# Performance work log

Measured on AMD Instinct MI355X. Metric: run time of the kernel, lower is better.

Reference implementation:

```python
import jax, jax.numpy as jnp
import numpy as np

H = 256
NUM_HEADS = 4
HEAD_DIM = H // NUM_HEADS


def _mlp(x, W1, b1, W2, b2):
    # Linear(2H->H) + ReLU + (dropout=identity in eval) + Linear(H->H)
    h = jax.nn.relu(x @ W1.T + b1)
    return h @ W2.T + b2


def setup_inputs() -> dict:
    key = jax.random.key(0)
    ks = jax.random.split(key, 24)
    s2h = 1.0 / np.sqrt(2 * H)
    sh = 1.0 / np.sqrt(H)
    inp = {
        'qubit_embeddings': jax.random.normal(ks[0], (65536, H), jnp.float32),
        'qpu_embeddings': jax.random.normal(ks[1], (64, H), jnp.float32),
        'gate_embeddings': jax.random.normal(ks[2], (65536, H), jnp.float32),
        'all_embeddings': jax.random.normal(ks[3], (131072, H), jnp.float32),
        'time_table': jax.random.normal(ks[4], (1000, H), jnp.float32),
        'map_W1': jax.random.normal(ks[5], (H, 2 * H), jnp.float32) * s2h,
        'map_b1': jnp.zeros((H,), jnp.float32),
        'map_W2': jax.random.normal(ks[6], (H, H), jnp.float32) * sh,
        'map_b2': jnp.zeros((H,), jnp.float32),
        'sch_W1': jax.random.normal(ks[7], (H, 2 * H), jnp.float32) * s2h,
        'sch_b1': jnp.zeros((H,), jnp.float32),
        'sch_W2': jax.random.normal(ks[8], (H, H), jnp.float32) * sh,
        'sch_b2': jnp.zeros((H,), jnp.float32),
        'qg_W1': jax.random.normal(ks[9], (H, H), jnp.float32) * sh,
        'qg_b1': jnp.zeros((H,), jnp.float32),
        'qg_W2': jax.random.normal(ks[10], (H, H), jnp.float32) * sh,
        'qg_b2': jnp.zeros((H,), jnp.float32),
        'attn_Wq': jax.random.normal(ks[11], (H, H), jnp.float32) * sh,
        'attn_bq': jnp.zeros((H,), jnp.float32),
        'attn_Wk': jax.random.normal(ks[12], (H, H), jnp.float32) * sh,
        'attn_bk': jnp.zeros((H,), jnp.float32),
        'attn_Wv': jax.random.normal(ks[13], (H, H), jnp.float32) * sh,
        'attn_bv': jnp.zeros((H,), jnp.float32),
        'attn_Wo': jax.random.normal(ks[14], (H, H), jnp.float32) * sh,
        'attn_bo': jnp.zeros((H,), jnp.float32),
        'map_qubit': jax.random.randint(ks[15], (131072,), 0, 65536, jnp.int32),
        'map_qpu': jax.random.randint(ks[16], (131072,), 0, 64, jnp.int32),
        'sched_gate': jax.random.randint(ks[17], (131072,), 0, 65536, jnp.int32),
        'sched_time': jax.random.randint(ks[18], (131072,), 0, 1000, jnp.int32),
    }
    return inp


def reference(qubit_embeddings, qpu_embeddings, gate_embeddings, all_embeddings,
              time_table, map_W1, map_b1, map_W2, map_b2,
              sch_W1, sch_b1, sch_W2, sch_b2,
              qg_W1, qg_b1, qg_W2, qg_b2,
              attn_Wq, attn_bq, attn_Wk, attn_bk, attn_Wv, attn_bv,
              attn_Wo, attn_bo,
              map_qubit, map_qpu, sched_gate, sched_time):
    # Vectorized form of the per-action Python loop: gather + concat + MLP.
    map_in = jnp.concatenate([qubit_embeddings[map_qubit], qpu_embeddings[map_qpu]], axis=-1)  # [Nm, 2H]
    map_keys = _mlp(map_in, map_W1, map_b1, map_W2, map_b2)                                    # [Nm, H]
    sch_in = jnp.concatenate([gate_embeddings[sched_gate], time_table[sched_time]], axis=-1)   # [Ns, 2H]
    sch_keys = _mlp(sch_in, sch_W1, sch_b1, sch_W2, sch_b2)                                    # [Ns, H]
    keys = jnp.concatenate([map_keys, sch_keys], axis=0)                                       # [A, H]

    g = all_embeddings.mean(axis=0)                                                            # [H]
    query = jax.nn.relu(g @ qg_W1.T + qg_b1) @ qg_W2.T + qg_b2                                 # [H]

    # MultiheadAttention: batch=1, q_len=1, kv_len=A (dropout=0 in eval, mask all-valid).
    q = (query @ attn_Wq.T + attn_bq).reshape(NUM_HEADS, HEAD_DIM)
    k = (keys @ attn_Wk.T + attn_bk).reshape(-1, NUM_HEADS, HEAD_DIM)
    v = (keys @ attn_Wv.T + attn_bv).reshape(-1, NUM_HEADS, HEAD_DIM)
    scores = jnp.einsum('hd,ahd->ha', q, k) / jnp.sqrt(jnp.asarray(HEAD_DIM, q.dtype))
    w = jax.nn.softmax(scores, axis=-1)                                                        # [heads, A]
    ctx = jnp.einsum('ha,ahd->hd', w, v).reshape(H)
    attn_out = ctx @ attn_Wo.T + attn_bo                                                       # [H]

    action_logits = keys @ attn_out                                                            # [A]
    action_probs = jax.nn.softmax(action_logits, axis=-1)
    return action_probs, action_logits
```

## Files before the change

kernel.cpp:

```cpp
#include <hip/hip_runtime.h>
#include <cstdint>
#include <cstddef>

typedef __bf16 bf16_t;
typedef __bf16 bf16x8 __attribute__((ext_vector_type(8)));
typedef __bf16 bf16x4 __attribute__((ext_vector_type(4)));
typedef __bf16 bf16x2 __attribute__((ext_vector_type(2)));
typedef float f32x4 __attribute__((ext_vector_type(4)));

#define A_TOTAL 262144
#define NMAP    131072

__global__ __launch_bounds__(256) void k_w1b16(
    const float* __restrict__ mW1, const float* __restrict__ sW1,
    bf16_t* __restrict__ dst) {
  int e = blockIdx.x * 256 + threadIdx.x;
  int slice = e >> 16, idx = e & 65535;
  int n = idx >> 8, k = idx & 255;
  float v;
  switch (slice) {
    case 0:  v = mW1[n * 512 + k]; break;
    case 1:  v = mW1[n * 512 + 256 + k]; break;
    case 2:  v = sW1[n * 512 + k]; break;
    default: v = sW1[n * 512 + 256 + k]; break;
  }
  dst[e] = (bf16_t)v;
}

__global__ __launch_bounds__(256) void k_w2ext(
    const float* __restrict__ mW2, const float* __restrict__ sW2,
    bf16_t* __restrict__ wext) {
  int row = blockIdx.x, tab = blockIdx.y, k = threadIdx.x;
  const float* W2 = tab ? sW2 : mW2;
  bf16_t v = (row < 256) ? (bf16_t)W2[row * 256 + k] : (bf16_t)0.f;
  wext[(size_t)tab * 272 * 256 + (size_t)row * 256 + k] = v;
}

__global__ __launch_bounds__(256) void k_mean(const float* __restrict__ A,
                                              float* __restrict__ part) {
  int t = threadIdx.x, b = blockIdx.x;
  const float* base = A + (size_t)b * 512 * 256 + t;
  float s = 0.f;
  for (int r = 0; r < 512; ++r) s += base[(size_t)r * 256];
  part[b * 256 + t] = s;
}

__global__ __launch_bounds__(256) void k_front(
    const float* __restrict__ meanPart,
    const float* __restrict__ qgW1, const float* __restrict__ qgb1,
    const float* __restrict__ qgW2, const float* __restrict__ qgb2,
    const float* __restrict__ Wq,  const float* __restrict__ bq,
    const float* __restrict__ Wk,
    const float* __restrict__ mW2, const float* __restrict__ sW2,
    bf16_t* __restrict__ wext) {
  __shared__ float g[256], h1[256], qry[256], qv[256];
  __shared__ float qks[4][256];
  int t = threadIdx.x;
  float s = 0.f;
  for (int b = 0; b < 256; ++b) s += meanPart[b * 256 + t];
  g[t] = s * (1.0f / 131072.0f);
  __syncthreads();
  {
    const f32x4* row = (const f32x4*)(qgW1 + (size_t)t * 256);
    float acc = 0.f;
    for (int k = 0; k < 64; ++k) {
      f32x4 w = row[k];
      acc += w[0] * g[4 * k] + w[1] * g[4 * k + 1] + w[2] * g[4 * k + 2] + w[3] * g[4 * k + 3];
    }
    h1[t] = fmaxf(acc + qgb1[t], 0.f);
  }
  __syncthreads();
  {
    const f32x4* row = (const f32x4*)(qgW2 + (size_t)t * 256);
    float acc = 0.f;
    for (int k = 0; k < 64; ++k) {
      f32x4 w = row[k];
      acc += w[0] * h1[4 * k] + w[1] * h1[4 * k + 1] + w[2] * h1[4 * k + 2] + w[3] * h1[4 * k + 3];
    }
    qry[t] = acc + qgb2[t];
  }
  __syncthreads();
  {
    const f32x4* row = (const f32x4*)(Wq + (size_t)t * 256);
    float acc = 0.f;
    for (int k = 0; k < 64; ++k) {
      f32x4 w = row[k];
      acc += w[0] * qry[4 * k] + w[1] * qry[4 * k + 1] + w[2] * qry[4 * k + 2] + w[3] * qry[4 * k + 3];
    }
    qv[t] = acc + bq[t];
  }
  __syncthreads();
  for (int h = 0; h < 4; ++h) {
    float acc = 0.f;
    for (int d = 0; d < 64; ++d) acc += qv[h * 64 + d] * Wk[(size_t)(h * 64 + d) * 256 + t];
    qks[h][t] = acc * 0.125f;
  }
  __syncthreads();
  for (int tab = 0; tab < 2; ++tab) {
    const float* W2 = tab ? sW2 : mW2;
    float acc0 = 0.f, acc1 = 0.f, acc2 = 0.f, acc3 = 0.f;
    for (int n = 0; n < 256; ++n) {
      float wv = W2[(size_t)n * 256 + t];
      acc0 += qks[0][n] * wv;
      acc1 += qks[1][n] * wv;
      acc2 += qks[2][n] * wv;
      acc3 += qks[3][n] * wv;
    }
    bf16_t* dst = wext + (size_t)tab * 272 * 256;
    dst[(256 + 0) * 256 + t] = (bf16_t)acc0;
    dst[(256 + 1) * 256 + t] = (bf16_t)acc1;
    dst[(256 + 2) * 256 + t] = (bf16_t)acc2;
    dst[(256 + 3) * 256 + t] = (bf16_t)acc3;
  }
}

__global__ __launch_bounds__(512, 4) void gemm_direct3(
    const float* __restrict__ A0, int M0, const bf16_t* __restrict__ W0,
    const float* __restrict__ b0, bf16_t* __restrict__ C0, int split,
    const float* __restrict__ A1, int M1, const bf16_t* __restrict__ W1,
    const float* __restrict__ b1, bf16_t* __restrict__ C1) {
  __shared__ __align__(16) bf16_t Xo[128][264];
  int blk = blockIdx.x;
  const float* A; int M; const bf16_t* W; const float* bias; bf16_t* C; int bid;
  if (blk < split) { A = A0; M = M0; W = W0; bias = b0; C = C0; bid = blk; }
  else             { A = A1; M = M1; W = W1; bias = b1; C = C1; bid = blk - split; }
  int t = threadIdx.x;
  int w = t >> 6, lane = t & 63;
  int lm = lane & 15, q = lane >> 4;
  int mloc0 = (w & 1) * 64;
  int m0 = bid * 128 + mloc0;
  int c0 = (w >> 1) * 64;
  int rows[4];
#pragma unroll
  for (int i = 0; i < 4; ++i) {
    int m = m0 + i * 16 + lm;
    rows[i] = m < M ? m : M - 1;
  }
  f32x4 acc[4][4] = {};
#pragma unroll
  for (int kt = 0; kt < 8; ++kt) {
    int k0 = kt * 32 + q * 8;
    bf16x8 b[4];
#pragma unroll
    for (int j = 0; j < 4; ++j)
      b[j] = *(const bf16x8*)(W + (size_t)(c0 + j * 16 + lm) * 256 + k0);
#pragma unroll
    for (int i = 0; i < 4; ++i) {
      const float* src = A + (size_t)rows[i] * 256 + k0;
      f32x4 lo = *(const f32x4*)src;
      f32x4 hi = *(const f32x4*)(src + 4);
      bf16x8 a;
#pragma unroll
      for (int x = 0; x < 4; ++x) { a[x] = (bf16_t)lo[x]; a[x + 4] = (bf16_t)hi[x]; }
#pragma unroll
      for (int j = 0; j < 4; ++j)
        acc[i][j] = __builtin_amdgcn_mfma_f32_16x16x32_bf16(a, b[j], acc[i][j], 0, 0, 0);
    }
  }
#pragma unroll
  for (int j = 0; j < 4; ++j) {
    int col = c0 + j * 16 + lm;
    float bb = bias ? bias[col] : 0.f;
#pragma unroll
    for (int i = 0; i < 4; ++i)
#pragma unroll
      for (int r = 0; r < 4; ++r)
        Xo[mloc0 + i * 16 + q * 4 + r][col] = (bf16_t)(acc[i][j][r] + bb);
  }
  __syncthreads();
  size_t tile0 = (size_t)bid * 128;
  const char* lds = (const char*)&Xo[0][0];
#pragma unroll
  for (int s = 0; s < 8; ++s) {
    int flat = s * 8192 + t * 16;
    int row = flat >> 9, colb = flat & 511;
    if (tile0 + (size_t)row < (size_t)M) {
      uint4 v = *(const uint4*)(lds + row * 528 + colb);
      *(uint4*)((char*)C + tile0 * 512 + (size_t)flat) = v;
    }
  }
}

__global__ __launch_bounds__(256, 4) void gemm_gather3(
    const bf16_t* __restrict__ Pa0, const bf16_t* __restrict__ Pb0,
    const int* __restrict__ idxA0, const int* __restrict__ idxB0,
    const bf16_t* __restrict__ Wext0, const float* __restrict__ bias0,
    const bf16_t* __restrict__ Pa1, const bf16_t* __restrict__ Pb1,
    const int* __restrict__ idxA1, const int* __restrict__ idxB1,
    const bf16_t* __restrict__ Wext1, const float* __restrict__ bias1,
    bf16_t* __restrict__ C,
    float* __restrict__ scores, float* __restrict__ partMax) {
  __shared__ __align__(16) bf16_t X[64][264];
  __shared__ float sred[4];
  int blk = blockIdx.x;
  int half = blk >> 11, bid = blk & 2047;
  const bf16_t* Pa; const bf16_t* Pb; const int* idxA; const int* idxB;
  const bf16_t* Wext; const float* bias;
  if (half == 0) { Pa = Pa0; Pb = Pb0; idxA = idxA0; idxB = idxB0; Wext = Wext0; bias = bias0; }
  else           { Pa = Pa1; Pb = Pb1; idxA = idxA1; idxB = idxB1; Wext = Wext1; bias = bias1; }
  int scoreBase = half * NMAP;
  int pmBase = half * 2048;

  int t = threadIdx.x;
  int w = t >> 6, lane = t & 63;
  int lm = lane & 15, q = lane >> 4;
  int cw = w * 64;
  int r = t >> 2, qa = t & 3;
  int row0 = bid * 64;
  int ia = idxA[row0 + r], ib = idxB[row0 + r];
  const bf16_t* paRow = Pa + (size_t)ia * 256;
  const bf16_t* pbRow = Pb + (size_t)ib * 256;

  bf16x8 va[8], vb[8];
#pragma unroll
  for (int s = 0; s < 8; ++s) {
    int ch = s * 4 + qa;
    va[s] = *(const bf16x8*)(paRow + ch * 8);
    vb[s] = *(const bf16x8*)(pbRow + ch * 8);
  }
#pragma unroll
  for (int s = 0; s < 8; ++s) {
    int ch = s * 4 + qa;
    bf16x8 x;
#pragma unroll
    for (int e = 0; e < 8; ++e)
      x[e] = (bf16_t)fmaxf((float)va[s][e] + (float)vb[s][e], 0.f);
    *(bf16x8*)&X[r][ch * 8] = x;
  }
  __syncthreads();

  f32x4 acc[4][4] = {};
  f32x4 accs[4] = {};
  bool doScore = (w == 0);
#pragma unroll
  for (int kt = 0; kt < 8; ++kt) {
    int kl = kt * 32 + q * 8;
    bf16x8 a[4];
#pragma unroll
    for (int i = 0; i < 4; ++i)
      a[i] = *(const bf16x8*)&X[i * 16 + lm][kl];
#pragma unroll
    for (int j = 0; j < 4; ++j) {
      bf16x8 b = *(const bf16x8*)(Wext + (size_t)(cw + j * 16 + lm) * 256 + kl);
#pragma unroll
      for (int i = 0; i < 4; ++i)
        acc[i][j] = __builtin_amdgcn_mfma_f32_16x16x32_bf16(a[i], b, acc[i][j], 0, 0, 0);
    }
    if (doScore) {
      bf16x8 bs = *(const bf16x8*)(Wext + (size_t)(256 + lm) * 256 + kl);
#pragma unroll
      for (int i = 0; i < 4; ++i)
        accs[i] = __builtin_amdgcn_mfma_f32_16x16x32_bf16(a[i], bs, accs[i], 0, 0, 0);
    }
  }
  __syncthreads();
#pragma unroll
  for (int j = 0; j < 4; ++j) {
    int col = cw + j * 16 + lm;
    float bb = bias[col];
#pragma unroll
    for (int i = 0; i < 4; ++i)
#pragma unroll
      for (int rr = 0; rr < 4; ++rr)
        X[i * 16 + q * 4 + rr][col] = (bf16_t)(acc[i][j][rr] + bb);
  }
  float hmax = -3.4e38f;
  if (doScore) {
    if (lm < 4) {
#pragma unroll
      for (int i = 0; i < 4; ++i)
#pragma unroll
        for (int rr = 0; rr < 4; ++rr) {
          int m = i * 16 + q * 4 + rr;
          float v = accs[i][rr];
          scores[(size_t)lm * A_TOTAL + scoreBase + row0 + m] = v;
          hmax = fmaxf(hmax, v);
        }
    }
    float m1 = fmaxf(hmax, __shfl_xor(hmax, 16));
    float m2 = fmaxf(m1, __shfl_xor(m1, 32));
    if (lane < 4) sred[lane] = m2;
  }
  __syncthreads();
  size_t gRow0 = (size_t)(half * NMAP + row0);
  const char* lds = (const char*)&X[0][0];
#pragma unroll
  for (int s = 0; s < 8; ++s) {
    int flat = s * 4096 + t * 16;
    int row = flat >> 9, colb = flat & 511;
    uint4 v = *(const uint4*)(lds + row * 528 + colb);
    *(uint4*)((char*)C + gRow0 * 512 + (size_t)flat) = v;
  }
  if (t < 4) partMax[t * 4096 + pmBase + bid] = sred[t];
}

__global__ __launch_bounds__(256) void k_smax2(const float* __restrict__ pM,
                                               float* __restrict__ Mh) {
  int t = threadIdx.x;
  __shared__ float red[256];
  for (int h = 0; h < 4; ++h) {
    float m = -3.4e38f;
    for (int i = t; i < 4096; i += 256) m = fmaxf(m, pM[h * 4096 + i]);
    red[t] = m;
    __syncthreads();
    for (int s = 128; s > 0; s >>= 1) {
      if (t < s) red[t] = fmaxf(red[t], red[t + s]);
      __syncthreads();
    }
    if (t == 0) Mh[h] = red[0];
    __syncthreads();
  }
}

__global__ __launch_bounds__(256) void k_ssum(const float* __restrict__ scores,
                                              const float* __restrict__ Mh,
                                              float* __restrict__ part) {
  int b = blockIdx.x, t = threadIdx.x;
  float m = Mh[b >> 6];
  const float* base = scores + (size_t)b * 4096;
  float s = 0.f;
  for (int i = 0; i < 16; ++i) s += __expf(base[i * 256 + t] - m);
  __shared__ float red[256];
  red[t] = s;
  __syncthreads();
  for (int st = 128; st > 0; st >>= 1) {
    if (t < st) red[t] += red[t + st];
    __syncthreads();
  }
  if (t == 0) part[b] = red[0];
}

__global__ __launch_bounds__(256) void k_ssum2(const float* __restrict__ part,
                                               float* __restrict__ invS) {
  int t = threadIdx.x;
  __shared__ float red[256];
  red[t] = part[t];
  __syncthreads();
  for (int s = 32; s > 0; s >>= 1) {
    if ((t & 63) < s) red[t] += red[t + s];
    __syncthreads();
  }
  if ((t & 63) == 0) invS[t >> 6] = 1.0f / red[t];
}

__global__ __launch_bounds__(256) void k_u(
    const bf16_t* __restrict__ keys, const float* __restrict__ scores,
    const float* __restrict__ Mh, const float* __restrict__ invS,
    float* __restrict__ u) {
  __shared__ float wl[4][512];
  __shared__ float uloc[8][4][256];
  int t = threadIdx.x;
  int a0 = blockIdx.x * 512;
#pragma unroll
  for (int i = 0; i < 8; ++i) {
    int e = i * 256 + t;
    int h = e >> 9, rr = e & 511;
    wl[h][rr] = __expf(scores[(size_t)h * A_TOTAL + a0 + rr] - Mh[h]) * invS[h];
  }
  __syncthreads();
  int tc = t & 31, rh = t >> 5;
  float acc[4][8] = {};
  for (int rr = 0; rr < 64; ++rr) {
    int al = rh * 64 + rr;
    bf16x8 kv = *(const bf16x8*)(keys + (size_t)(a0 + al) * 256 + tc * 8);
    float f[8];
#pragma unroll
    for (int e = 0; e < 8; ++e) f[e] = (float)kv[e];
#pragma unroll
    for (int h = 0; h < 4; ++h) {
      float wv = wl[h][al];
#pragma unroll
      for (int e = 0; e < 8; ++e) acc[h][e] += wv * f[e];
    }
  }
#pragma unroll
  for (int h = 0; h < 4; ++h)
#pragma unroll
    for (int e = 0; e < 8; ++e) uloc[rh][h][tc * 8 + e] = acc[h][e];
  __syncthreads();
#pragma unroll
  for (int h = 0; h < 4; ++h) {
    float v = 0.f;
#pragma unroll
    for (int g = 0; g < 8; ++g) v += uloc[g][h][t];
    atomicAdd(&u[h * 256 + t], v);
  }
}

__global__ __launch_bounds__(256) void k_attn(
    const float* __restrict__ u, const float* __restrict__ Wv,
    const float* __restrict__ bv, const float* __restrict__ Wo,
    const float* __restrict__ bo, float* __restrict__ attn_out,
    bf16_t* __restrict__ attn_pad) {
  __shared__ float ctx[256];
  int t = threadIdx.x;
  int h = t >> 6;
  const float* uh = u + h * 256;
  {
    const f32x4* row = (const f32x4*)(Wv + (size_t)t * 256);
    float acc = 0.f;
    for (int k = 0; k < 64; ++k) {
      f32x4 w = row[k];
      acc += w[0] * uh[4 * k] + w[1] * uh[4 * k + 1] + w[2] * uh[4 * k + 2] + w[3] * uh[4 * k + 3];
    }
    ctx[t] = acc + bv[t];
  }
  __syncthreads();
  {
    const f32x4* row = (const f32x4*)(Wo + (size_t)t * 256);
    float acc = 0.f;
    for (int k = 0; k < 64; ++k) {
      f32x4 w = row[k];
      acc += w[0] * ctx[4 * k] + w[1] * ctx[4 * k + 1] + w[2] * ctx[4 * k + 2] + w[3] * ctx[4 * k + 3];
    }
    float v = acc + bo[t];
    attn_out[t] = v;
    attn_pad[t] = (bf16_t)v;
#pragma unroll
    for (int i = 1; i < 16; ++i) attn_pad[i * 256 + t] = (bf16_t)0.f;
  }
}

__global__ __launch_bounds__(256) void k_logits2(
    const bf16_t* __restrict__ keys, const bf16_t* __restrict__ attn_pad,
    float* __restrict__ out_logits, float* __restrict__ blockMax) {
  int t = threadIdx.x;
  int w = t >> 6, lane = t & 63;
  int lm = lane & 15, q = lane >> 4;
  int m0 = blockIdx.x * 256 + w * 64;
  bf16x8 b[8];
#pragma unroll
  for (int kt = 0; kt < 8; ++kt)
    b[kt] = *(const bf16x8*)(attn_pad + lm * 256 + kt * 32 + q * 8);
  f32x4 acc[4] = {};
#pragma unroll
  for (int i = 0; i < 4; ++i) {
    const bf16_t* arow = keys + (size_t)(m0 + i * 16 + lm) * 256 + q * 8;
#pragma unroll
    for (int kt = 0; kt < 8; ++kt) {
      bf16x8 a = *(const bf16x8*)(arow + kt * 32);
      acc[i] = __builtin_amdgcn_mfma_f32_16x16x32_bf16(a, b[kt], acc[i], 0, 0, 0);
    }
  }
  float lmax = -3.4e38f;
  if (lm == 0) {
#pragma unroll
    for (int i = 0; i < 4; ++i) {
      *(f32x4*)(out_logits + m0 + i * 16 + q * 4) = acc[i];
#pragma unroll
      for (int rr = 0; rr < 4; ++rr) lmax = fmaxf(lmax, acc[i][rr]);
    }
  }
  float m1 = fmaxf(lmax, __shfl_xor(lmax, 16));
  float m2 = fmaxf(m1, __shfl_xor(m1, 32));
  __shared__ float red[4];
  if (lane == 0) red[w] = m2;
  __syncthreads();
  if (t == 0)
    blockMax[blockIdx.x] = fmaxf(fmaxf(red[0], red[1]), fmaxf(red[2], red[3]));
}

__global__ __launch_bounds__(256) void k_lred1(const float* __restrict__ bm,
                                               float* __restrict__ Ml) {
  int t = threadIdx.x;
  float m = -3.4e38f;
  for (int i = t; i < 1024; i += 256) m = fmaxf(m, bm[i]);
  __shared__ float red[256];
  red[t] = m;
  __syncthreads();
  for (int s = 128; s > 0; s >>= 1) {
    if (t < s) red[t] = fmaxf(red[t], red[t + s]);
    __syncthreads();
  }
  if (t == 0) Ml[0] = red[0];
}

__global__ __launch_bounds__(256) void k_lsum(const float* __restrict__ logits,
                                              const float* __restrict__ Ml,
                                              float* __restrict__ part) {
  int t = threadIdx.x, b = blockIdx.x;
  float m = Ml[0];
  float s = __expf(logits[b * 512 + t] - m) + __expf(logits[b * 512 + 256 + t] - m);
  __shared__ float red[256];
  red[t] = s;
  __syncthreads();
  for (int st = 128; st > 0; st >>= 1) {
    if (t < st) red[t] += red[t + st];
    __syncthreads();
  }
  if (t == 0) part[b] = red[0];
}

__global__ __launch_bounds__(256) void k_lred2(const float* __restrict__ part,
                                               float* __restrict__ invSl) {
  int t = threadIdx.x;
  float s = part[t] + part[t + 256];
  __shared__ float red[256];
  red[t] = s;
  __syncthreads();
  for (int st = 128; st > 0; st >>= 1) {
    if (t < st) red[t] += red[t + st];
    __syncthreads();
  }
  if (t == 0) invSl[0] = 1.0f / red[0];
}

__global__ __launch_bounds__(256) void k_probs(const float* __restrict__ logits,
                                               const float* __restrict__ Ml,
                                               const float* __restrict__ invSl,
                                               float* __restrict__ probs) {
  int i = blockIdx.x * 256 + threadIdx.x;
  probs[i] = __expf(logits[i] - Ml[0]) * invSl[0];
}

extern "C" void kernel_launch(void* const* d_in, const int* in_sizes, int n_in,
                              void* d_out, int out_size, void* d_ws, size_t ws_size,
                              hipStream_t stream) {
  const float* qubit_emb = (const float*)d_in[0];
  const float* qpu_emb   = (const float*)d_in[1];
  const float* gate_emb  = (const float*)d_in[2];
  const float* all_emb   = (const float*)d_in[3];
  const float* time_tab  = (const float*)d_in[4];
  const float* map_W1 = (const float*)d_in[5];
  const float* map_b1 = (const float*)d_in[6];
  const float* map_W2 = (const float*)d_in[7];
  const float* map_b2 = (const float*)d_in[8];
  const float* sch_W1 = (const float*)d_in[9];
  const float* sch_b1 = (const float*)d_in[10];
  const float* sch_W2 = (const float*)d_in[11];
  const float* sch_b2 = (const float*)d_in[12];
  const float* qg_W1 = (const float*)d_in[13];
  const float* qg_b1 = (const float*)d_in[14];
  const float* qg_W2 = (const float*)d_in[15];
  const float* qg_b2 = (const float*)d_in[16];
  const float* Wq = (const float*)d_in[17];
  const float* bq = (const float*)d_in[18];
  const float* Wk = (const float*)d_in[19];
  const float* Wv = (const float*)d_in[21];
  const float* bv = (const float*)d_in[22];
  const float* Wo = (const float*)d_in[23];
  const float* bo = (const float*)d_in[24];
  const int* map_qubit  = (const int*)d_in[25];
  const int* map_qpu    = (const int*)d_in[26];
  const int* sched_gate = (const int*)d_in[27];
  const int* sched_time = (const int*)d_in[28];
  (void)in_sizes; (void)n_in; (void)out_size;

  char* ws = (char*)d_ws;
  size_t off = 0;
  auto alloc = [&](size_t b) { size_t r = off; off += (b + 255) & ~(size_t)255; return r; };
  size_t KEYS  = alloc((size_t)A_TOTAL * 256 * 2);
  size_t PQ    = alloc((size_t)65536 * 256 * 2);
  size_t PG    = alloc((size_t)65536 * 256 * 2);
  size_t PP    = alloc((size_t)128 * 256 * 2);
  size_t PT    = alloc((size_t)1024 * 256 * 2);
  size_t W1B   = alloc((size_t)4 * 65536 * 2);
  size_t WEXT  = alloc((size_t)2 * 272 * 256 * 2);
  size_t SCORE = alloc((size_t)4 * A_TOTAL * 4);
  size_t MPART = alloc((size_t)256 * 256 * 4);
  size_t APAD  = alloc((size_t)16 * 256 * 2);
  size_t ATTN  = alloc(256 * 4);
  size_t U     = alloc(4 * 256 * 4);
  size_t PMAX  = alloc(4 * 4096 * 4);
  size_t MH    = alloc(4 * 4);
  size_t SINV  = alloc(4 * 4);
  size_t BMAX  = alloc(1024 * 4);
  size_t ML    = alloc(4);
  size_t SLINV = alloc(4);
  size_t LPART = alloc(512 * 4);
  size_t SPART = alloc(256 * 4);
  if (off > ws_size) return;

  bf16_t* keysP  = (bf16_t*)(ws + KEYS);
  bf16_t* pqP    = (bf16_t*)(ws + PQ);
  bf16_t* pgP    = (bf16_t*)(ws + PG);
  bf16_t* ppP    = (bf16_t*)(ws + PP);
  bf16_t* ptP    = (bf16_t*)(ws + PT);
  bf16_t* w1bP   = (bf16_t*)(ws + W1B);
  bf16_t* wextP  = (bf16_t*)(ws + WEXT);
  float*  scoreP = (float*)(ws + SCORE);
  float*  mpartP = (float*)(ws + MPART);
  bf16_t* apadP  = (bf16_t*)(ws + APAD);
  float*  attnP  = (float*)(ws + ATTN);
  float*  uP     = (float*)(ws + U);
  float*  pmaxP  = (float*)(ws + PMAX);
  float*  mhP    = (float*)(ws + MH);
  float*  sinvP  = (float*)(ws + SINV);
  float*  bmaxP  = (float*)(ws + BMAX);
  float*  mlP    = (float*)(ws + ML);
  float*  slinvP = (float*)(ws + SLINV);
  float*  lpartP = (float*)(ws + LPART);
  float*  spartP = (float*)(ws + SPART);

  float* probsOut  = (float*)d_out;
  float* logitsOut = probsOut + A_TOTAL;

  hipMemsetAsync(uP, 0, 4 * 256 * 4, stream);

  k_w1b16<<<1024, 256, 0, stream>>>(map_W1, sch_W1, w1bP);
  k_w2ext<<<dim3(272, 2), 256, 0, stream>>>(map_W2, sch_W2, wextP);
  k_mean<<<256, 256, 0, stream>>>(all_emb, mpartP);
  k_front<<<1, 256, 0, stream>>>(mpartP, qg_W1, qg_b1, qg_W2, qg_b2,
                                 Wq, bq, Wk, map_W2, sch_W2, wextP);

  gemm_direct3<<<1024, 512, 0, stream>>>(
      qubit_emb, 65536, w1bP + 0 * 65536, nullptr, pqP, 512,
      gate_emb,  65536, w1bP + 2 * 65536, nullptr, pgP);
  gemm_direct3<<<9, 512, 0, stream>>>(
      qpu_emb, 64,   w1bP + 1 * 65536, map_b1, ppP, 1,
      time_tab, 1000, w1bP + 3 * 65536, sch_b1, ptP);

  gemm_gather3<<<4096, 256, 0, stream>>>(
      pqP, ppP, map_qubit, map_qpu, wextP, map_b2,
      pgP, ptP, sched_gate, sched_time, wextP + 272 * 256, sch_b2,
      keysP, scoreP, pmaxP);

  k_smax2<<<1, 256, 0, stream>>>(pmaxP, mhP);
  k_ssum<<<256, 256, 0, stream>>>(scoreP, mhP, spartP);
  k_ssum2<<<1, 256, 0, stream>>>(spartP, sinvP);

  k_u<<<512, 256, 0, stream>>>(keysP, scoreP, mhP, sinvP, uP);
  k_attn<<<1, 256, 0, stream>>>(uP, Wv, bv, Wo, bo, attnP, apadP);

  k_logits2<<<1024, 256, 0, stream>>>(keysP, apadP, logitsOut, bmaxP);
  k_lred1<<<1, 256, 0, stream>>>(bmaxP, mlP);
  k_lsum<<<512, 256, 0, stream>>>(logitsOut, mlP, lpartP);
  k_lred2<<<1, 256, 0, stream>>>(lpartP, slinvP);
  k_probs<<<1024, 256, 0, stream>>>(logitsOut, mlP, slinvP, probsOut);
}
```

Baseline: 754.6 us.

## Fuse reduction tail kernels via last-block atomics and gather rows directly from global

```diff
diff --git a/kernel.cpp b/kernel.cpp
--- a/kernel.cpp
+++ b/kernel.cpp
@@ -11,37 +11,40 @@
 #define A_TOTAL 262144
 #define NMAP    131072
 
-__global__ __launch_bounds__(256) void k_w1b16(
+__global__ __launch_bounds__(256) void k_prep(
     const float* __restrict__ mW1, const float* __restrict__ sW1,
-    bf16_t* __restrict__ dst) {
-  int e = blockIdx.x * 256 + threadIdx.x;
-  int slice = e >> 16, idx = e & 65535;
-  int n = idx >> 8, k = idx & 255;
-  float v;
-  switch (slice) {
-    case 0:  v = mW1[n * 512 + k]; break;
-    case 1:  v = mW1[n * 512 + 256 + k]; break;
-    case 2:  v = sW1[n * 512 + k]; break;
-    default: v = sW1[n * 512 + 256 + k]; break;
-  }
-  dst[e] = (bf16_t)v;
-}
-
-__global__ __launch_bounds__(256) void k_w2ext(
+    bf16_t* __restrict__ w1b,
     const float* __restrict__ mW2, const float* __restrict__ sW2,
     bf16_t* __restrict__ wext) {
-  int row = blockIdx.x, tab = blockIdx.y, k = threadIdx.x;
-  const float* W2 = tab ? sW2 : mW2;
-  bf16_t v = (row < 256) ? (bf16_t)W2[row * 256 + k] : (bf16_t)0.f;
-  wext[(size_t)tab * 272 * 256 + (size_t)row * 256 + k] = v;
+  int b = blockIdx.x, t = threadIdx.x;
+  if (b < 1024) {
+    int e = b * 256 + t;
+    int slice = e >> 16, idx = e & 65535;
+    int n = idx >> 8, k = idx & 255;
+    float v;
+    switch (slice) {
+      case 0:  v = mW1[n * 512 + k]; break;
+      case 1:  v = mW1[n * 512 + 256 + k]; break;
+      case 2:  v = sW1[n * 512 + k]; break;
+      default: v = sW1[n * 512 + 256 + k]; break;
+    }
+    w1b[e] = (bf16_t)v;
+  } else {
+    int e2 = b - 1024;
+    int tab = e2 >= 272 ? 1 : 0;
+    int row = e2 - tab * 272;
+    const float* W2 = tab ? sW2 : mW2;
+    bf16_t v = (row < 256) ? (bf16_t)W2[row * 256 + t] : (bf16_t)0.f;
+    wext[(size_t)tab * 272 * 256 + (size_t)row * 256 + t] = v;
+  }
 }
 
 __global__ __launch_bounds__(256) void k_mean(const float* __restrict__ A,
                                               float* __restrict__ part) {
   int t = threadIdx.x, b = blockIdx.x;
-  const float* base = A + (size_t)b * 512 * 256 + t;
+  const float* base = A + (size_t)b * 256 * 256 + t;
   float s = 0.f;
-  for (int r = 0; r < 512; ++r) s += base[(size_t)r * 256];
+  for (int r = 0; r < 256; ++r) s += base[(size_t)r * 256];
   part[b * 256 + t] = s;
 }
 
@@ -57,7 +60,7 @@
   __shared__ float qks[4][256];
   int t = threadIdx.x;
   float s = 0.f;
-  for (int b = 0; b < 256; ++b) s += meanPart[b * 256 + t];
+  for (int b = 0; b < 512; ++b) s += meanPart[b * 256 + t];
   g[t] = s * (1.0f / 131072.0f);
   __syncthreads();
   {
@@ -181,7 +184,7 @@
   }
 }
 
-__global__ __launch_bounds__(256, 4) void gemm_gather3(
+__global__ __launch_bounds__(256, 4) void gemm_gather4(
     const bf16_t* __restrict__ Pa0, const bf16_t* __restrict__ Pb0,
     const int* __restrict__ idxA0, const int* __restrict__ idxB0,
     const bf16_t* __restrict__ Wext0, const float* __restrict__ bias0,
@@ -189,86 +192,81 @@
     const int* __restrict__ idxA1, const int* __restrict__ idxB1,
     const bf16_t* __restrict__ Wext1, const float* __restrict__ bias1,
     bf16_t* __restrict__ C,
-    float* __restrict__ scores, float* __restrict__ partMax) {
-  __shared__ __align__(16) bf16_t X[64][264];
+    float* __restrict__ scores, float* __restrict__ partMax,
+    int* __restrict__ cnt, float* __restrict__ Mh) {
+  __shared__ __align__(16) bf16_t Xo[32][264];
   __shared__ float sred[4];
+  __shared__ int isLast;
   int blk = blockIdx.x;
-  int half = blk >> 11, bid = blk & 2047;
+  int half = blk >> 12, bid = blk & 4095;
   const bf16_t* Pa; const bf16_t* Pb; const int* idxA; const int* idxB;
   const bf16_t* Wext; const float* bias;
   if (half == 0) { Pa = Pa0; Pb = Pb0; idxA = idxA0; idxB = idxB0; Wext = Wext0; bias = bias0; }
   else           { Pa = Pa1; Pb = Pb1; idxA = idxA1; idxB = idxB1; Wext = Wext1; bias = bias1; }
   int scoreBase = half * NMAP;
-  int pmBase = half * 2048;
+  int pmBase = half * 4096;
 
   int t = threadIdx.x;
   int w = t >> 6, lane = t & 63;
   int lm = lane & 15, q = lane >> 4;
   int cw = w * 64;
-  int r = t >> 2, qa = t & 3;
-  int row0 = bid * 64;
-  int ia = idxA[row0 + r], ib = idxB[row0 + r];
-  const bf16_t* paRow = Pa + (size_t)ia * 256;
-  const bf16_t* pbRow = Pb + (size_t)ib * 256;
-
-  bf16x8 va[8], vb[8];
-#pragma unroll
-  for (int s = 0; s < 8; ++s) {
-    int ch = s * 4 + qa;
-    va[s] = *(const bf16x8*)(paRow + ch * 8);
-    vb[s] = *(const bf16x8*)(pbRow + ch * 8);
-  }
-#pragma unroll
-  for (int s = 0; s < 8; ++s) {
-    int ch = s * 4 + qa;
-    bf16x8 x;
-#pragma unroll
-    for (int e = 0; e < 8; ++e)
-      x[e] = (bf16_t)fmaxf((float)va[s][e] + (float)vb[s][e], 0.f);
-    *(bf16x8*)&X[r][ch * 8] = x;
-  }
-  __syncthreads();
-
-  f32x4 acc[4][4] = {};
-  f32x4 accs[4] = {};
+  int row0 = bid * 32;
+
+  const bf16_t* pa[2]; const bf16_t* pb[2];
+#pragma unroll
+  for (int i = 0; i < 2; ++i) {
+    int r = row0 + i * 16 + lm;
+    pa[i] = Pa + (size_t)idxA[r] * 256 + q * 8;
+    pb[i] = Pb + (size_t)idxB[r] * 256 + q * 8;
+  }
+
+  f32x4 acc[2][4] = {};
+  f32x4 accs[2] = {};
   bool doScore = (w == 0);
 #pragma unroll
   for (int kt = 0; kt < 8; ++kt) {
-    int kl = kt * 32 + q * 8;
-    bf16x8 a[4];
-#pragma unroll
-    for (int i = 0; i < 4; ++i)
-      a[i] = *(const bf16x8*)&X[i * 16 + lm][kl];
+    int kc = kt * 32;
+    int kq = kc + q * 8;
+    bf16x8 a[2];
+#pragma unroll
+    for (int i = 0; i < 2; ++i) {
+      bf16x8 va = *(const bf16x8*)(pa[i] + kc);
+      bf16x8 vb = *(const bf16x8*)(pb[i] + kc);
+      bf16x8 x;
+#pragma unroll
+      for (int e = 0; e < 8; ++e)
+        x[e] = (bf16_t)fmaxf((float)va[e] + (float)vb[e], 0.f);
+      a[i] = x;
+    }
 #pragma unroll
     for (int j = 0; j < 4; ++j) {
-      bf16x8 b = *(const bf16x8*)(Wext + (size_t)(cw + j * 16 + lm) * 256 + kl);
-#pragma unroll
-      for (int i = 0; i < 4; ++i)
+      bf16x8 b = *(const bf16x8*)(Wext + (size_t)(cw + j * 16 + lm) * 256 + kq);
+#pragma unroll
+      for (int i = 0; i < 2; ++i)
         acc[i][j] = __builtin_amdgcn_mfma_f32_16x16x32_bf16(a[i], b, acc[i][j], 0, 0, 0);
     }
     if (doScore) {
-      bf16x8 bs = *(const bf16x8*)(Wext + (size_t)(256 + lm) * 256 + kl);
-#pragma unroll
-      for (int i = 0; i < 4; ++i)
+      bf16x8 bs = *(const bf16x8*)(Wext + (size_t)(256 + lm) * 256 + kq);
+#pragma unroll
+      for (int i = 0; i < 2; ++i)
         accs[i] = __builtin_amdgcn_mfma_f32_16x16x32_bf16(a[i], bs, accs[i], 0, 0, 0);
     }
   }
-  __syncthreads();
 #pragma unroll
   for (int j = 0; j < 4; ++j) {
     int col = cw + j * 16 + lm;
     float bb = bias[col];
 #pragma unroll
-    for (int i = 0; i < 4; ++i)
+    for (int i = 0; i < 2; ++i)
 #pragma unroll
       for (int rr = 0; rr < 4; ++rr)
-        X[i * 16 + q * 4 + rr][col] = (bf16_t)(acc[i][j][rr] + bb);
+        Xo[i * 16 + q * 4 + rr][col] = (bf16_t)(acc[i][j][rr] + bb);
   }
   float hmax = -3.4e38f;
   if (doScore) {
     if (lm < 4) {
 #pragma unroll
-      for (int i = 0; i < 4; ++i)
+      for (int i = 0; i < 2; ++i)
 #pragma unroll
         for (int rr = 0; rr < 4; ++rr) {
           int m = i * 16 + q * 4 + rr;
@@ -283,24 +281,25 @@
   }
   __syncthreads();
   size_t gRow0 = (size_t)(half * NMAP + row0);
-  const char* lds = (const char*)&X[0][0];
-#pragma unroll
-  for (int s = 0; s < 8; ++s) {
+  const char* lds = (const char*)&Xo[0][0];
+#pragma unroll
+  for (int s = 0; s < 4; ++s) {
     int flat = s * 4096 + t * 16;
     int row = flat >> 9, colb = flat & 511;
     uint4 v = *(const uint4*)(lds + row * 528 + colb);
     *(uint4*)((char*)C + gRow0 * 512 + (size_t)flat) = v;
   }
-  if (t < 4) partMax[t * 4096 + pmBase + bid] = sred[t];
-}
-
-__global__ __launch_bounds__(256) void k_smax2(const float* __restrict__ pM,
-                                               float* __restrict__ Mh) {
-  int t = threadIdx.x;
-  __shared__ float red[256];
+  if (t < 4) partMax[t * 8192 + pmBase + bid] = sred[t];
+  __threadfence();
+  __syncthreads();
+  if (t == 0) isLast = (atomicAdd(cnt, 1) == (int)gridDim.x - 1);
+  __syncthreads();
+  if (!isLast) return;
+  __threadfence();
+  float* red = (float*)&Xo[0][0];
   for (int h = 0; h < 4; ++h) {
     float m = -3.4e38f;
-    for (int i = t; i < 4096; i += 256) m = fmaxf(m, pM[h * 4096 + i]);
+    for (int i = t; i < 8192; i += 256) m = fmaxf(m, partMax[h * 8192 + i]);
     red[t] = m;
     __syncthreads();
     for (int s = 128; s > 0; s >>= 1) {
@@ -312,52 +311,34 @@
   }
 }
 
-__global__ __launch_bounds__(256) void k_ssum(const float* __restrict__ scores,
-                                              const float* __restrict__ Mh,
-                                              float* __restrict__ part) {
-  int b = blockIdx.x, t = threadIdx.x;
-  float m = Mh[b >> 6];
-  const float* base = scores + (size_t)b * 4096;
-  float s = 0.f;
-  for (int i = 0; i < 16; ++i) s += __expf(base[i * 256 + t] - m);
-  __shared__ float red[256];
-  red[t] = s;
-  __syncthreads();
-  for (int st = 128; st > 0; st >>= 1) {
-    if (t < st) red[t] += red[t + st];
-    __syncthreads();
-  }
-  if (t == 0) part[b] = red[0];
-}
-
-__global__ __launch_bounds__(256) void k_ssum2(const float* __restrict__ part,
-                                               float* __restrict__ invS) {
-  int t = threadIdx.x;
-  __shared__ float red[256];
-  red[t] = part[t];
-  __syncthreads();
-  for (int s = 32; s > 0; s >>= 1) {
-    if ((t & 63) < s) red[t] += red[t + s];
-    __syncthreads();
-  }
-  if ((t & 63) == 0) invS[t >> 6] = 1.0f / red[t];
-}
-
-__global__ __launch_bounds__(256) void k_u(
+__global__ __launch_bounds__(256) void k_u2(
     const bf16_t* __restrict__ keys, const float* __restrict__ scores,
-    const float* __restrict__ Mh, const float* __restrict__ invS,
-    float* __restrict__ u) {
+    const float* __restrict__ Mh,
+    float* __restrict__ u, float* __restrict__ Ssum, int* __restrict__ cnt,
+    const float* __restrict__ Wv, const float* __restrict__ bv,
+    const float* __restrict__ Wo, const float* __restrict__ bo,
+    bf16_t* __restrict__ attn_pad) {
   __shared__ float wl[4][512];
   __shared__ float uloc[8][4][256];
+  __shared__ int isLast;
   int t = threadIdx.x;
   int a0 = blockIdx.x * 512;
 #pragma unroll
   for (int i = 0; i < 8; ++i) {
     int e = i * 256 + t;
     int h = e >> 9, rr = e & 511;
-    wl[h][rr] = __expf(scores[(size_t)h * A_TOTAL + a0 + rr] - Mh[h]) * invS[h];
-  }
-  __syncthreads();
+    wl[h][rr] = __expf(scores[(size_t)h * A_TOTAL + a0 + rr] - Mh[h]);
+  }
+  __syncthreads();
+  {
+    int h = t >> 6, l = t & 63;
+    float s = 0.f;
+#pragma unroll
+    for (int j = 0; j < 8; ++j) s += wl[h][l + j * 64];
+#pragma unroll
+    for (int o = 32; o > 0; o >>= 1) s += __shfl_xor(s, o);
+    if (l == 0) atomicAdd(&Ssum[h], s);
+  }
   int tc = t & 31, rh = t >> 5;
   float acc[4][8] = {};
   for (int rr = 0; rr < 64; ++rr) {
@@ -385,45 +366,48 @@
     for (int g = 0; g < 8; ++g) v += uloc[g][h][t];
     atomicAdd(&u[h * 256 + t], v);
   }
-}
-
-__global__ __launch_bounds__(256) void k_attn(
-    const float* __restrict__ u, const float* __restrict__ Wv,
-    const float* __restrict__ bv, const float* __restrict__ Wo,
-    const float* __restrict__ bo, float* __restrict__ attn_out,
-    bf16_t* __restrict__ attn_pad) {
-  __shared__ float ctx[256];
-  int t = threadIdx.x;
+  __threadfence();
+  __syncthreads();
+  if (t == 0) isLast = (atomicAdd(cnt, 1) == (int)gridDim.x - 1);
+  __syncthreads();
+  if (!isLast) return;
+  __threadfence();
+  float* ctx = &wl[0][0];
   int h = t >> 6;
-  const float* uh = u + h * 256;
   {
+    float invS = 1.0f / Ssum[h];
     const f32x4* row = (const f32x4*)(Wv + (size_t)t * 256);
-    float acc = 0.f;
+    const f32x4* uh  = (const f32x4*)(u + h * 256);
+    float acc2 = 0.f;
     for (int k = 0; k < 64; ++k) {
       f32x4 w = row[k];
-      acc += w[0] * uh[4 * k] + w[1] * uh[4 * k + 1] + w[2] * uh[4 * k + 2] + w[3] * uh[4 * k + 3];
-    }
-    ctx[t] = acc + bv[t];
+      f32x4 x = uh[k];
+      acc2 += w[0] * x[0] + w[1] * x[1] + w[2] * x[2] + w[3] * x[3];
+    }
+    ctx[t] = acc2 * invS + bv[t];
   }
   __syncthreads();
   {
     const f32x4* row = (const f32x4*)(Wo + (size_t)t * 256);
-    float acc = 0.f;
+    float acc2 = 0.f;
     for (int k = 0; k < 64; ++k) {
       f32x4 w = row[k];
-      acc += w[0] * ctx[4 * k] + w[1] * ctx[4 * k + 1] + w[2] * ctx[4 * k + 2] + w[3] * ctx[4 * k + 3];
-    }
-    float v = acc + bo[t];
-    attn_out[t] = v;
+      acc2 += w[0] * ctx[4 * k] + w[1] * ctx[4 * k + 1] + w[2] * ctx[4 * k + 2] + w[3] * ctx[4 * k + 3];
+    }
+    float v = acc2 + bo[t];
     attn_pad[t] = (bf16_t)v;
 #pragma unroll
     for (int i = 1; i < 16; ++i) attn_pad[i * 256 + t] = (bf16_t)0.f;
   }
 }
 
-__global__ __launch_bounds__(256) void k_logits2(
+__global__ __launch_bounds__(256) void k_logits3(
     const bf16_t* __restrict__ keys, const bf16_t* __restrict__ attn_pad,
-    float* __restrict__ out_logits, float* __restrict__ blockMax) {
+    float* __restrict__ out_logits, float* __restrict__ blockMax,
+    int* __restrict__ cnt, float* __restrict__ Ml) {
+  __shared__ float red[4];
+  __shared__ float red2[256];
+  __shared__ int isLast;
   int t = threadIdx.x;
   int w = t >> 6, lane = t & 63;
   int lm = lane & 15, q = lane >> 4;
@@ -453,50 +437,53 @@
   }
   float m1 = fmaxf(lmax, __shfl_xor(lmax, 16));
   float m2 = fmaxf(m1, __shfl_xor(m1, 32));
-  __shared__ float red[4];
   if (lane == 0) red[w] = m2;
   __syncthreads();
-  if (t == 0)
+  if (t == 0) {
     blockMax[blockIdx.x] = fmaxf(fmaxf(red[0], red[1]), fmaxf(red[2], red[3]));
-}
-
-__global__ __launch_bounds__(256) void k_lred1(const float* __restrict__ bm,
-                                               float* __restrict__ Ml) {
-  int t = threadIdx.x;
+    __threadfence();
+    isLast = (atomicAdd(cnt, 1) == (int)gridDim.x - 1);
+  }
+  __syncthreads();
+  if (!isLast) return;
+  __threadfence();
   float m = -3.4e38f;
-  for (int i = t; i < 1024; i += 256) m = fmaxf(m, bm[i]);
+  for (int i = t; i < 1024; i += 256) m = fmaxf(m, blockMax[i]);
+  red2[t] = m;
+  __syncthreads();
+  for (int s = 128; s > 0; s >>= 1) {
+    if (t < s) red2[t] = fmaxf(red2[t], red2[t + s]);
+    __syncthreads();
+  }
+  if (t == 0) Ml[0] = red2[0];
+}
+
+__global__ __launch_bounds__(256) void k_lsum2(const float* __restrict__ logits,
+                                               const float* __restrict__ Ml,
+                                               float* __restrict__ part,
+                                               int* __restrict__ cnt,
+                                               float* __restrict__ invSl) {
+  int t = threadIdx.x, b = blockIdx.x;
   __shared__ float red[256];
-  red[t] = m;
-  __syncthreads();
-  for (int s = 128; s > 0; s >>= 1) {
-    if (t < s) red[t] = fmaxf(red[t], red[t + s]);
-    __syncthreads();
-  }
-  if (t == 0) Ml[0] = red[0];
-}
-
-__global__ __launch_bounds__(256) void k_lsum(const float* __restrict__ logits,
-                                              const float* __restrict__ Ml,
-                                              float* __restrict__ part) {
-  int t = threadIdx.x, b = blockIdx.x;
+  __shared__ int isLast;
   float m = Ml[0];
   float s = __expf(logits[b * 512 + t] - m) + __expf(logits[b * 512 + 256 + t] - m);
-  __shared__ float red[256];
   red[t] = s;
   __syncthreads();
   for (int st = 128; st > 0; st >>= 1) {
     if (t < st) red[t] += red[t + st];
     __syncthreads();
   }
-  if (t == 0) part[b] = red[0];
-}
-
-__global__ __launch_bounds__(256) void k_lred2(const float* __restrict__ part,
-                                               float* __restrict__ invSl) {
-  int t = threadIdx.x;
-  float s = part[t] + part[t + 256];
-  __shared__ float red[256];
-  red[t] = s;
+  if (t == 0) {
+    part[b] = red[0];
+    __threadfence();
+    isLast = (atomicAdd(cnt, 1) == (int)gridDim.x - 1);
+  }
+  __syncthreads();
+  if (!isLast) return;
+  __threadfence();
+  float v = part[t] + part[t + 256];
+  red[t] = v;
   __syncthreads();
   for (int st = 128; st > 0; st >>= 1) {
     if (t < st) red[t] += red[t + st];
@@ -557,18 +544,17 @@
   size_t W1B   = alloc((size_t)4 * 65536 * 2);
   size_t WEXT  = alloc((size_t)2 * 272 * 256 * 2);
   size_t SCORE = alloc((size_t)4 * A_TOTAL * 4);
-  size_t MPART = alloc((size_t)256 * 256 * 4);
+  size_t MPART = alloc((size_t)512 * 256 * 4);
   size_t APAD  = alloc((size_t)16 * 256 * 2);
-  size_t ATTN  = alloc(256 * 4);
   size_t U     = alloc(4 * 256 * 4);
-  size_t PMAX  = alloc(4 * 4096 * 4);
+  size_t SSUM  = alloc(4 * 4);
+  size_t CNT   = alloc(4 * 4);
+  size_t PMAX  = alloc(4 * 8192 * 4);
   size_t MH    = alloc(4 * 4);
-  size_t SINV  = alloc(4 * 4);
   size_t BMAX  = alloc(1024 * 4);
   size_t ML    = alloc(4);
   size_t SLINV = alloc(4);
   size_t LPART = alloc(512 * 4);
-  size_t SPART = alloc(256 * 4);
   if (off > ws_size) return;
 
   bf16_t* keysP  = (bf16_t*)(ws + KEYS);
@@ -581,25 +567,23 @@
   float*  scoreP = (float*)(ws + SCORE);
   float*  mpartP = (float*)(ws + MPART);
   bf16_t* apadP  = (bf16_t*)(ws + APAD);
-  float*  attnP  = (float*)(ws + ATTN);
   float*  uP     = (float*)(ws + U);
+  float*  ssumP  = (float*)(ws + SSUM);
+  int*    cntP   = (int*)(ws + CNT);
   float*  pmaxP  = (float*)(ws + PMAX);
   float*  mhP    = (float*)(ws + MH);
-  float*  sinvP  = (float*)(ws + SINV);
   float*  bmaxP  = (float*)(ws + BMAX);
   float*  mlP    = (float*)(ws + ML);
   float*  slinvP = (float*)(ws + SLINV);
   float*  lpartP = (float*)(ws + LPART);
-  float*  spartP = (float*)(ws + SPART);
 
   float* probsOut  = (float*)d_out;
   float* logitsOut = probsOut + A_TOTAL;
 
-  hipMemsetAsync(uP, 0, 4 * 256 * 4, stream);
-
-  k_w1b16<<<1024, 256, 0, stream>>>(map_W1, sch_W1, w1bP);
-  k_w2ext<<<dim3(272, 2), 256, 0, stream>>>(map_W2, sch_W2, wextP);
-  k_mean<<<256, 256, 0, stream>>>(all_emb, mpartP);
+  hipMemsetAsync(uP, 0, 4608, stream);
+
+  k_prep<<<1568, 256, 0, stream>>>(map_W1, sch_W1, w1bP, map_W2, sch_W2, wextP);
+  k_mean<<<512, 256, 0, stream>>>(all_emb, mpartP);
   k_front<<<1, 256, 0, stream>>>(mpartP, qg_W1, qg_b1, qg_W2, qg_b2,
                                  Wq, bq, Wk, map_W2, sch_W2, wextP);
 
@@ -610,21 +594,16 @@
       qpu_emb, 64,   w1bP + 1 * 65536, map_b1, ppP, 1,
       time_tab, 1000, w1bP + 3 * 65536, sch_b1, ptP);
 
-  gemm_gather3<<<4096, 256, 0, stream>>>(
+  gemm_gather4<<<8192, 256, 0, stream>>>(
       pqP, ppP, map_qubit, map_qpu, wextP, map_b2,
       pgP, ptP, sched_gate, sched_time, wextP + 272 * 256, sch_b2,
-      keysP, scoreP, pmaxP);
-
-  k_smax2<<<1, 256, 0, stream>>>(pmaxP, mhP);
-  k_ssum<<<256, 256, 0, stream>>>(scoreP, mhP, spartP);
-  k_ssum2<<<1, 256, 0, stream>>>(spartP, sinvP);
-
-  k_u<<<512, 256, 0, stream>>>(keysP, scoreP, mhP, sinvP, uP);
-  k_attn<<<1, 256, 0, stream>>>(uP, Wv, bv, Wo, bo, attnP, apadP);
-
-  k_logits2<<<1024, 256, 0, stream>>>(keysP, apadP, logitsOut, bmaxP);
-  k_lred1<<<1, 256, 0, stream>>>(bmaxP, mlP);
-  k_lsum<<<512, 256, 0, stream>>>(logitsOut, mlP, lpartP);
-  k_lred2<<<1, 256, 0, stream>>>(lpartP, slinvP);
+      keysP, scoreP, pmaxP, cntP + 0, mhP);
+
+  k_u2<<<512, 256, 0, stream>>>(keysP, scoreP, mhP, uP, ssumP, cntP + 1,
+                                Wv, bv, Wo, bo, apadP);
+
+  k_logits3<<<1024, 256, 0, stream>>>(keysP, apadP, logitsOut, bmaxP,
+                                      cntP + 2, mlP);
+  k_lsum2<<<512, 256, 0, stream>>>(logitsOut, mlP, lpartP, cntP + 3, slinvP);
   k_probs<<<1024, 256, 0, stream>>>(logitsOut, mlP, slinvP, probsOut);
 }
```

Measured after the change: 1.844 ms. +144.3%, slower.

## Make gather-GEMM persistent over four 32-row tiles with prefetched gathers

Applied to the files above, without the earlier changes.

```diff
diff --git a/kernel.cpp b/kernel.cpp
--- a/kernel.cpp
+++ b/kernel.cpp
@@ -181,7 +181,7 @@
   }
 }
 
-__global__ __launch_bounds__(256, 4) void gemm_gather3(
+__global__ __launch_bounds__(256, 4) void gemm_gather5(
     const bf16_t* __restrict__ Pa0, const bf16_t* __restrict__ Pb0,
     const int* __restrict__ idxA0, const int* __restrict__ idxB0,
     const bf16_t* __restrict__ Wext0, const float* __restrict__ bias0,
@@ -190,108 +190,131 @@
     const bf16_t* __restrict__ Wext1, const float* __restrict__ bias1,
     bf16_t* __restrict__ C,
     float* __restrict__ scores, float* __restrict__ partMax) {
-  __shared__ __align__(16) bf16_t X[64][264];
+  __shared__ __align__(16) bf16_t X[32][264];
   __shared__ float sred[4];
-  int blk = blockIdx.x;
-  int half = blk >> 11, bid = blk & 2047;
-  const bf16_t* Pa; const bf16_t* Pb; const int* idxA; const int* idxB;
-  const bf16_t* Wext; const float* bias;
-  if (half == 0) { Pa = Pa0; Pb = Pb0; idxA = idxA0; idxB = idxB0; Wext = Wext0; bias = bias0; }
-  else           { Pa = Pa1; Pb = Pb1; idxA = idxA1; idxB = idxB1; Wext = Wext1; bias = bias1; }
-  int scoreBase = half * NMAP;
-  int pmBase = half * 2048;
-
   int t = threadIdx.x;
   int w = t >> 6, lane = t & 63;
   int lm = lane & 15, q = lane >> 4;
   int cw = w * 64;
-  int r = t >> 2, qa = t & 3;
-  int row0 = bid * 64;
-  int ia = idxA[row0 + r], ib = idxB[row0 + r];
-  const bf16_t* paRow = Pa + (size_t)ia * 256;
-  const bf16_t* pbRow = Pb + (size_t)ib * 256;
-
-  bf16x8 va[8], vb[8];
-#pragma unroll
-  for (int s = 0; s < 8; ++s) {
-    int ch = s * 4 + qa;
-    va[s] = *(const bf16x8*)(paRow + ch * 8);
-    vb[s] = *(const bf16x8*)(pbRow + ch * 8);
-  }
-#pragma unroll
-  for (int s = 0; s < 8; ++s) {
-    int ch = s * 4 + qa;
-    bf16x8 x;
-#pragma unroll
-    for (int e = 0; e < 8; ++e)
-      x[e] = (bf16_t)fmaxf((float)va[s][e] + (float)vb[s][e], 0.f);
-    *(bf16x8*)&X[r][ch * 8] = x;
-  }
-  __syncthreads();
-
-  f32x4 acc[4][4] = {};
-  f32x4 accs[4] = {};
-  bool doScore = (w == 0);
-#pragma unroll
-  for (int kt = 0; kt < 8; ++kt) {
-    int kl = kt * 32 + q * 8;
-    bf16x8 a[4];
-#pragma unroll
-    for (int i = 0; i < 4; ++i)
-      a[i] = *(const bf16x8*)&X[i * 16 + lm][kl];
+  int r = t >> 3, qa = t & 7;
+  int b = blockIdx.x;
+
+  bf16x8 va[4], vb[4];
+  {
+    int ia = idxA0[b * 32 + r], ib = idxB0[b * 32 + r];
+    const bf16_t* paRow = Pa0 + (size_t)ia * 256;
+    const bf16_t* pbRow = Pb0 + (size_t)ib * 256;
+#pragma unroll
+    for (int s = 0; s < 4; ++s) {
+      int ch = s * 8 + qa;
+      va[s] = *(const bf16x8*)(paRow + ch * 8);
+      vb[s] = *(const bf16x8*)(pbRow + ch * 8);
+    }
+  }
+  int ian = 0, ibn = 0;
+
+#pragma unroll
+  for (int it = 0; it < 4; ++it) {
+    const int half = it >> 1;
+    const int bid  = b + (it & 1) * 2048;
+    const int row0 = bid * 32;
+    const bf16_t* Wext = half ? Wext1 : Wext0;
+    const float*  bias = half ? bias1 : bias0;
+
+    if (it < 3) {
+      const int bidn = b + ((it + 1) & 1) * 2048;
+      const int* iA = ((it + 1) < 2) ? idxA0 : idxA1;
+      const int* iB = ((it + 1) < 2) ? idxB0 : idxB1;
+      ian = iA[bidn * 32 + r];
+      ibn = iB[bidn * 32 + r];
+    }
+    if (it) __syncthreads();
+#pragma unroll
+    for (int s = 0; s < 4; ++s) {
+      int ch = s * 8 + qa;
+      bf16x8 x;
+#pragma unroll
+      for (int e = 0; e < 8; ++e)
+        x[e] = (bf16_t)fmaxf((float)va[s][e] + (float)vb[s][e], 0.f);
+      *(bf16x8*)&X[r][ch * 8] = x;
+    }
+    __syncthreads();
+    if (it < 3) {
+      const bf16_t* Pan = ((it + 1) < 2) ? Pa0 : Pa1;
+      const bf16_t* Pbn = ((it + 1) < 2) ? Pb0 : Pb1;
+      const bf16_t* paRow = Pan + (size_t)ian * 256;
+      const bf16_t* pbRow = Pbn + (size_t)ibn * 256;
+#pragma unroll
+      for (int s = 0; s < 4; ++s) {
+        int ch = s * 8 + qa;
+        va[s] = *(const bf16x8*)(paRow + ch * 8);
+        vb[s] = *(const bf16x8*)(pbRow + ch * 8);
+      }
+    }
+    f32x4 acc[2][4] = {};
+    f32x4 accs[2] = {};
+    bool doScore = (w == 0);
+#pragma unroll
+    for (int kt = 0; kt < 8; ++kt) {
+      int kl = kt * 32 + q * 8;
+      bf16x8 a[2];
+#pragma unroll
+      for (int i = 0; i < 2; ++i)
+        a[i] = *(const bf16x8*)&X[i * 16 + lm][kl];
+#pragma unroll
+      for (int j = 0; j < 4; ++j) {
+        bf16x8 bw = *(const bf16x8*)(Wext + (size_t)(cw + j * 16 + lm) * 256 + kl);
+#pragma unroll
+        for (int i = 0; i < 2; ++i)
+          acc[i][j] = __builtin_amdgcn_mfma_f32_16x16x32_bf16(a[i], bw, acc[i][j], 0, 0, 0);
+      }
+      if (doScore) {
+        bf16x8 bs = *(const bf16x8*)(Wext + (size_t)(256 + lm) * 256 + kl);
+#pragma unroll
+        for (int i = 0; i < 2; ++i)
+          accs[i] = __builtin_amdgcn_mfma_f32_16x16x32_bf16(a[i], bs, accs[i], 0, 0, 0);
+      }
+    }
+    __syncthreads();
 #pragma unroll
     for (int j = 0; j < 4; ++j) {
-      bf16x8 b = *(const bf16x8*)(Wext + (size_t)(cw + j * 16 + lm) * 256 + kl);
-#pragma unroll
-      for (int i = 0; i < 4; ++i)
-        acc[i][j] = __builtin_amdgcn_mfma_f32_16x16x32_bf16(a[i], b, acc[i][j], 0, 0, 0);
-    }
+      int col = cw + j * 16 + lm;
+      float bb = bias[col];
+#pragma unroll
+      for (int i = 0; i < 2; ++i)
+#pragma unroll
+        for (int rr = 0; rr < 4; ++rr)
+          X[i * 16 + q * 4 + rr][col] = (bf16_t)(acc[i][j][rr] + bb);
+    }
+    float hmax = -3.4e38f;
     if (doScore) {
-      bf16x8 bs = *(const bf16x8*)(Wext + (size_t)(256 + lm) * 256 + kl);
-#pragma unroll
-      for (int i = 0; i < 4; ++i)
-        accs[i] = __builtin_amdgcn_mfma_f32_16x16x32_bf16(a[i], bs, accs[i], 0, 0, 0);
-    }
-  }
-  __syncthreads();
-#pragma unroll
-  for (int j = 0; j < 4; ++j) {
-    int col = cw + j * 16 + lm;
-    float bb = bias[col];
-#pragma unroll
-    for (int i = 0; i < 4; ++i)
-#pragma unroll
-      for (int rr = 0; rr < 4; ++rr)
-        X[i * 16 + q * 4 + rr][col] = (bf16_t)(acc[i][j][rr] + bb);
-  }
-  float hmax = -3.4e38f;
-  if (doScore) {
-    if (lm < 4) {
-#pragma unroll
-      for (int i = 0; i < 4; ++i)
-#pragma unroll
-        for (int rr = 0; rr < 4; ++rr) {
-          int m = i * 16 + q * 4 + rr;
-          float v = accs[i][rr];
-          scores[(size_t)lm * A_TOTAL + scoreBase + row0 + m] = v;
-          hmax = fmaxf(hmax, v);
-        }
-    }
-    float m1 = fmaxf(hmax, __shfl_xor(hmax, 16));
-    float m2 = fmaxf(m1, __shfl_xor(m1, 32));
-    if (lane < 4) sred[lane] = m2;
-  }
-  __syncthreads();
-  size_t gRow0 = (size_t)(half * NMAP + row0);
-  const char* lds = (const char*)&X[0][0];
-#pragma unroll
-  for (int s = 0; s < 8; ++s) {
-    int flat = s * 4096 + t * 16;
-    int row = flat >> 9, colb = flat & 511;
-    uint4 v = *(const uint4*)(lds + row * 528 + colb);
-    *(uint4*)((char*)C + gRow0 * 512 + (size_t)flat) = v;
-  }
-  if (t < 4) partMax[t * 4096 + pmBase + bid] = sred[t];
+      if (lm < 4) {
+#pragma unroll
+        for (int i = 0; i < 2; ++i)
+#pragma unroll
+          for (int rr = 0; rr < 4; ++rr) {
+            int m = i * 16 + q * 4 + rr;
+            float v = accs[i][rr];
+            scores[(size_t)lm * A_TOTAL + half * NMAP + row0 + m] = v;
+            hmax = fmaxf(hmax, v);
+          }
+      }
+      float m1 = fmaxf(hmax, __shfl_xor(hmax, 16));
+      float m2 = fmaxf(m1, __shfl_xor(m1, 32));
+      if (lane < 4) sred[lane] = m2;
+    }
+    __syncthreads();
+    size_t gRow0 = (size_t)(half * NMAP + row0);
+    const char* lds = (const char*)&X[0][0];
+#pragma unroll
+    for (int s = 0; s < 4; ++s) {
+      int flat = s * 4096 + t * 16;
+      int row = flat >> 9, colb = flat & 511;
+      uint4 v = *(const uint4*)(lds + row * 528 + colb);
+      *(uint4*)((char*)C + gRow0 * 512 + (size_t)flat) = v;
+    }
+    if (t < 4) partMax[t * 8192 + half * 4096 + bid] = sred[t];
+  }
 }
 
 __global__ __launch_bounds__(256) void k_smax2(const float* __restrict__ pM,
@@ -300,7 +323,7 @@
   __shared__ float red[256];
   for (int h = 0; h < 4; ++h) {
     float m = -3.4e38f;
-    for (int i = t; i < 4096; i += 256) m = fmaxf(m, pM[h * 4096 + i]);
+    for (int i = t; i < 8192; i += 256) m = fmaxf(m, pM[h * 8192 + i]);
     red[t] = m;
     __syncthreads();
     for (int s = 128; s > 0; s >>= 1) {
@@ -561,7 +584,7 @@
   size_t APAD  = alloc((size_t)16 * 256 * 2);
   size_t ATTN  = alloc(256 * 4);
   size_t U     = alloc(4 * 256 * 4);
-  size_t PMAX  = alloc(4 * 4096 * 4);
+  size_t PMAX  = alloc(4 * 8192 * 4);
   size_t MH    = alloc(4 * 4);
   size_t SINV  = alloc(4 * 4);
   size_t BMAX  = alloc(1024 * 4);
@@ -610,7 +633,7 @@
       qpu_emb, 64,   w1bP + 1 * 65536, map_b1, ppP, 1,
       time_tab, 1000, w1bP + 3 * 65536, sch_b1, ptP);
 
-  gemm_gather3<<<4096, 256, 0, stream>>>(
+  gemm_gather5<<<2048, 256, 0, stream>>>(
       pqP, ppP, map_qubit, map_qpu, wextP, map_b2,
       pgP, ptP, sched_gate, sched_time, wextP + 272 * 256, sch_b2,
       keysP, scoreP, pmaxP);
```

New measurement: 840.7 us. 1.11x slower.
